# Optimization experiments

Hardware: AMD Instinct MI355X
Metric: run time of the kernel (lower is better)

Reference implementation:

```python
import jax, jax.numpy as jnp
import numpy as np

GAMMA = 0.95        # gamma_lemma: persistence decay per cycle (eq. 12.1)
KAPPA = 0.1         # kappa_interfere: lateral interference strength (eq. 12.3)
T_STEPS = 50        # t_lemma_steps: integration window before selection (eq. 12.2)
FLOOR = 1e-6        # confidence_floor for peak-to-average ratio

B, N_CONCEPTS, N_LEMMAS = 4096, 1024, 512


def setup_inputs() -> dict:
    key = jax.random.key(0)
    k1, k2 = jax.random.split(key, 2)
    # kernel boundary hands in a normalized concept distribution
    c_raw = jax.random.uniform(k1, (B, N_CONCEPTS), dtype=jnp.float32)
    c_lex = c_raw / jnp.sum(c_raw, axis=-1, keepdims=True)
    # TiedSubstrate W_C_to_L: (out_dim=n_lemmas, in_dim=n_concepts)
    W = jax.random.normal(k2, (N_LEMMAS, N_CONCEPTS), dtype=jnp.float32) / np.sqrt(N_CONCEPTS)
    # persistent lemma activation buffer a_lemma, zero at reset
    a0 = jnp.zeros((B, N_LEMMAS), dtype=jnp.float32)
    return {"c_lex": c_lex, "W": W, "a0": a0}


def reference(c_lex, W, a0):
    """Integrate lemma activations for T_STEPS cycles, then select.

    Per cycle (eq. 12.1 + 12.3):
      a <- gamma * a + c_lex @ W^T            # decay + concept->lemma drive
      a <- a - kappa * (sum_j a_j - a)        # lateral interference from other lemmas
      a <- max(a, 0)                          # rectify activations
    Selection (eq. 12.2): argmax over lemmas; confidence = peak / max(mean, floor).
    """
    def step(a, _):
        a = GAMMA * a + jnp.einsum('bc,lc->bl', c_lex, W)   # (B, n_lemmas)
        a = a - KAPPA * (jnp.sum(a, axis=-1, keepdims=True) - a)
        a = jnp.maximum(a, 0.0)
        return a, None

    a, _ = jax.lax.scan(step, a0, None, length=T_STEPS)
    peak = jnp.max(a, axis=-1)
    mean = jnp.mean(a, axis=-1)
    confidence = peak / jnp.maximum(mean, FLOOR)
    selected = jnp.argmax(a, axis=-1)
    return a, selected, confidence
```

## Files before the change

kernel.cpp:

```cpp
#include <hip/hip_runtime.h>
#include <hip/hip_bf16.h>

#define BATCH 4096
#define NC    1024
#define NL    512
#define TSTEPS 50
#define GAMMA_C 0.95f
#define KAPPA_C 0.1f
#define FLOOR_C 1e-6f

typedef __attribute__((ext_vector_type(8))) short short8;
typedef __attribute__((ext_vector_type(4))) float f32x4;

__device__ __forceinline__ void split2_pk(float x0, float x1,
                                          unsigned& hp, unsigned& lp) {
    union { __hip_bfloat162 b; unsigned u; } ch, cl;
    ch.b = __float22bfloat162_rn(make_float2(x0, x1));
    hp = ch.u;
    const float hf0 = __uint_as_float(hp << 16);
    const float hf1 = __uint_as_float(hp & 0xFFFF0000u);
    cl.b = __float22bfloat162_rn(make_float2(x0 - hf0, x1 - hf1));
    lp = cl.u;
}

__device__ __forceinline__ float wave_sum_bcast(float x) {
    float f = x;
    f += __int_as_float(__builtin_amdgcn_update_dpp(
            0, __float_as_int(f), 0x111, 0xf, 0xf, true));
    f += __int_as_float(__builtin_amdgcn_update_dpp(
            0, __float_as_int(f), 0x112, 0xf, 0xf, true));
    f += __int_as_float(__builtin_amdgcn_update_dpp(
            0, __float_as_int(f), 0x114, 0xf, 0xf, true));
    f += __int_as_float(__builtin_amdgcn_update_dpp(
            0, __float_as_int(f), 0x118, 0xf, 0xf, true));
    f += __int_as_float(__builtin_amdgcn_update_dpp(
            0, __float_as_int(f), 0x142, 0xa, 0xf, true));
    f += __int_as_float(__builtin_amdgcn_update_dpp(
            0, __float_as_int(f), 0x143, 0xc, 0xf, true));
    return __int_as_float(__builtin_amdgcn_readlane(__float_as_int(f), 63));
}

__device__ __forceinline__ void glds16f(const float* g, float* l) {
    __builtin_amdgcn_global_load_lds(
        (__attribute__((address_space(1))) void*)(g),
        (__attribute__((address_space(3))) void*)(l), 16, 0, 0);
}

#define TM 128
#define TN 128
#define GK 32
#define SPLITK 4
#define NST (NC / SPLITK / GK)

__global__ __launch_bounds__(256)
void gemm_f32stage(const float* __restrict__ A, const float* __restrict__ W,
                   float* __restrict__ Dp) {
    __shared__ float S[2][2][TM * GK];

    const int tid  = threadIdx.x;
    const int lane = tid & 63;
    const int w    = tid >> 6;

    const int b    = blockIdx.x;
    const int xcd  = b & 7;
    const int slot = b >> 3;
    const int mi_b = xcd * 4 + (slot & 3);
    const int nk   = slot >> 2;
    const int ni_b = nk & 3;
    const int kz   = nk >> 2;

    const int m0 = mi_b * TM;
    const int n0 = ni_b * TN;
    const int kb = kz * (NC / SPLITK);

    const int srow = lane >> 3;
    const int scol = ((lane & 7) * 4) ^ ((srow & 7) << 2);
    const float* gA = A + (size_t)(m0 + w * 32 + srow) * NC + kb + scol;
    const float* gB = W + (size_t)(n0 + w * 32 + srow) * NC + kb + scol;
    const int ldd = (w * 32) * GK;

    const int mw   = (w >> 1) * 64;
    const int nw   = (w & 1) * 64;
    const int sr   = lane & 15;
    const int quad = lane >> 4;
    const int swz = (sr & 7) << 2;
    const int c0  = (quad * 8) ^ swz;
    const int c1  = (quad * 8 + 4) ^ swz;
    const int rAo = (mw + sr) * GK;
    const int rBo = (nw + sr) * GK;

    f32x4 acc[4][4];
    #pragma unroll
    for (int i = 0; i < 4; ++i)
        #pragma unroll
        for (int j = 0; j < 4; ++j)
            acc[i][j] = (f32x4){0.f, 0.f, 0.f, 0.f};

    #define STAGE(buf, kofs)                                               \
        {                                                                  \
            const int ko = (kofs);                                         \
            _Pragma("unroll")                                              \
            for (int c = 0; c < 4; ++c) {                                  \
                glds16f(gA + (size_t)(c * 8) * NC + ko,                    \
                        &S[buf][0][ldd + c * 8 * GK]);                     \
                glds16f(gB + (size_t)(c * 8) * NC + ko,                    \
                        &S[buf][1][ldd + c * 8 * GK]);                     \
            }                                                              \
        }

    #define FRAG(ARR, ROFF, FH, FL)                                        \
        {                                                                  \
            const float4 f0 = *(const float4*)&S[CUR][ARR][(ROFF) + c0];   \
            const float4 f1 = *(const float4*)&S[CUR][ARR][(ROFF) + c1];   \
            uint4 hh, ll;                                                  \
            split2_pk(f0.x, f0.y, hh.x, ll.x);                             \
            split2_pk(f0.z, f0.w, hh.y, ll.y);                             \
            split2_pk(f1.x, f1.y, hh.z, ll.z);                             \
            split2_pk(f1.z, f1.w, hh.w, ll.w);                             \
            FH = *(const short8*)&hh;                                      \
            FL = *(const short8*)&ll;                                      \
        }

    #define KSTEP(CURV, VMSTR, DO_STAGE, NEXTK)                                \
        {                                                                      \
            const int CUR = (CURV);                                            \
            asm volatile("s_waitcnt vmcnt(" VMSTR ")" ::: "memory");           \
            __builtin_amdgcn_sched_barrier(0);                                 \
            __builtin_amdgcn_s_barrier();                                      \
            __builtin_amdgcn_sched_barrier(0);                                 \
            short8 afh[4], afl[4], bfh[4], bfl[4];                             \
            _Pragma("unroll")                                                  \
            for (int mi = 0; mi < 4; ++mi)                                     \
                FRAG(0, rAo + mi * 16 * GK, afh[mi], afl[mi]);                 \
            _Pragma("unroll")                                                  \
            for (int ni = 0; ni < 4; ++ni)                                     \
                FRAG(1, rBo + ni * 16 * GK, bfh[ni], bfl[ni]);                 \
            _Pragma("unroll")                                                  \
            for (int mi = 0; mi < 4; ++mi) {                                   \
                _Pragma("unroll")                                              \
                for (int ni = 0; ni < 4; ++ni) {                               \
                    acc[mi][ni] = __builtin_amdgcn_mfma_f32_16x16x32_bf16(     \
                        afh[mi], bfh[ni], acc[mi][ni], 0, 0, 0);               \
                    acc[mi][ni] = __builtin_amdgcn_mfma_f32_16x16x32_bf16(     \
                        afh[mi], bfl[ni], acc[mi][ni], 0, 0, 0);               \
                    acc[mi][ni] = __builtin_amdgcn_mfma_f32_16x16x32_bf16(     \
                        afl[mi], bfh[ni], acc[mi][ni], 0, 0, 0);               \
                }                                                              \
            }                                                                  \
            __builtin_amdgcn_sched_barrier(0);                                 \
            __builtin_amdgcn_s_barrier();                                      \
            __builtin_amdgcn_sched_barrier(0);                                 \
            if (DO_STAGE) STAGE(CUR, NEXTK);                                   \
        }

    STAGE(0, 0);
    STAGE(1, GK);

    #pragma unroll 2
    for (int s = 0; s < NST - 2; ++s)
        KSTEP((s & 1), "8", true, (s + 2) * GK);
    KSTEP(0, "8", false, 0);
    KSTEP(1, "0", false, 0);

    float* Dz = Dp + (size_t)kz * BATCH * NL;
    #pragma unroll
    for (int mi = 0; mi < 4; ++mi) {
        #pragma unroll
        for (int ni = 0; ni < 4; ++ni) {
            const int col = n0 + nw + ni * 16 + sr;
            #pragma unroll
            for (int r = 0; r < 4; ++r) {
                const int row = m0 + mw + mi * 16 + quad * 4 + r;
                Dz[(size_t)row * NL + col] = acc[mi][ni][r];
            }
        }
    }
}

template<int SK>
__global__ __launch_bounds__(256)
void iterate_select(const float* __restrict__ Dp,
                    float* __restrict__ a_out,
                    float* __restrict__ sel_out, float* __restrict__ conf_out) {
    const int lane = threadIdx.x & 63;
    const int wave = threadIdx.x >> 6;
    const int row  = blockIdx.x * 4 + wave;

    float d[8];
    {
        float4 v[SK][2];
        #pragma unroll
        for (int s = 0; s < SK; ++s) {
            const float4* ps = (const float4*)(Dp + (size_t)s * BATCH * NL
                                               + (size_t)row * NL + lane * 8);
            v[s][0] = ps[0];
            v[s][1] = ps[1];
        }
        d[0] = v[0][0].x; d[1] = v[0][0].y; d[2] = v[0][0].z; d[3] = v[0][0].w;
        d[4] = v[0][1].x; d[5] = v[0][1].y; d[6] = v[0][1].z; d[7] = v[0][1].w;
        #pragma unroll
        for (int s = 1; s < SK; ++s) {
            d[0] += v[s][0].x; d[1] += v[s][0].y; d[2] += v[s][0].z; d[3] += v[s][0].w;
            d[4] += v[s][1].x; d[5] += v[s][1].y; d[6] += v[s][1].z; d[7] += v[s][1].w;
        }
    }

    float a[8];
    #pragma unroll
    for (int j = 0; j < 8; ++j) a[j] = 0.f;

    const float K1 = 1.0f + KAPPA_C;

    for (int t = 0; t < TSTEPS; ++t) {
        #pragma unroll
        for (int j = 0; j < 8; ++j) a[j] = fmaf(GAMMA_C, a[j], d[j]);

        float t4a = a[0] + a[4], t4b = a[1] + a[5], t4c = a[2] + a[6], t4d = a[3] + a[7];
        float t2a = t4a + t4c, t2b = t4b + t4d;
        const float S = wave_sum_bcast(t2a + t2b);

        const float h = -KAPPA_C * S;
        #pragma unroll
        for (int j = 0; j < 8; ++j) {
            const float v = fmaf(K1, a[j], h);
            a[j] = v > 0.f ? v : 0.f;
        }
    }

    float m4a = fmaxf(a[0], a[4]), m4b = fmaxf(a[1], a[5]);
    float m4c = fmaxf(a[2], a[6]), m4d = fmaxf(a[3], a[7]);
    float peak = fmaxf(fmaxf(m4a, m4b), fmaxf(m4c, m4d));
    float s4a = a[0] + a[4], s4b = a[1] + a[5], s4c = a[2] + a[6], s4d = a[3] + a[7];
    float ssum = wave_sum_bcast((s4a + s4b) + (s4c + s4d));

    #pragma unroll
    for (int m = 1; m < 64; m <<= 1)
        peak = fmaxf(peak, __shfl_xor(peak, m, 64));

    const float mean = ssum * (1.0f / (float)NL);
    const float conf = peak / fmaxf(mean, FLOOR_C);

    int idx = 0x7fffffff;
    #pragma unroll
    for (int j = 0; j < 8; ++j)
        if (a[j] == peak) idx = min(idx, lane * 8 + j);
    #pragma unroll
    for (int m = 1; m < 64; m <<= 1)
        idx = min(idx, __shfl_xor(idx, m, 64));

    float4* ar = (float4*)(a_out + (size_t)row * NL + lane * 8);
    float4 o0, o1;
    o0.x = a[0]; o0.y = a[1]; o0.z = a[2]; o0.w = a[3];
    o1.x = a[4]; o1.y = a[5]; o1.z = a[6]; o1.w = a[7];
    ar[0] = o0; ar[1] = o1;

    if (lane == 0) {
        if (sel_out)  sel_out[row]  = (float)idx;
        if (conf_out) conf_out[row] = conf;
    }
}

extern "C" void kernel_launch(void* const* d_in, const int* in_sizes, int n_in,
                              void* d_out, int out_size, void* d_ws, size_t ws_size,
                              hipStream_t stream) {
    const float* c_lex = (const float*)d_in[0];
    const float* W     = (const float*)d_in[1];

    float* D = (float*)d_ws;

    float* a_out = (float*)d_out;
    float* sel   = nullptr;
    float* conf  = nullptr;
    const int base = BATCH * NL;
    if (out_size >= base + 2 * BATCH) {
        sel  = a_out + base;
        conf = a_out + base + BATCH;
    } else if (out_size >= base + BATCH) {
        conf = a_out + base;
    }

    gemm_f32stage<<<dim3(512), 256, 0, stream>>>(c_lex, W, D);

    iterate_select<SPLITK><<<dim3(BATCH / 4), 256, 0, stream>>>(D, a_out, sel, conf);
}
```

Before: 107.9 us.

## Fuse split-K GEMM and iteration into one cooperative kernel with grid sync

Merges the GEMM and the per-row iteration/selection into a single cooperative launch of 512 blocks, separated by a grid-wide sync, so there is one kernel launch instead of two. After the sync each block handles 8 rows, two per wave, instead of the previous 4 rows per block over 1024 blocks. If the cooperative launch fails it falls back to the two-kernel path. The grid sync and the lower row-level parallelism in the second phase (fewer waves in flight for the latency-bound 50-step loop) could offset the saved launch gap.

```diff
diff --git a/kernel.cpp b/kernel.cpp
--- a/kernel.cpp
+++ b/kernel.cpp
@@ -1,5 +1,8 @@
 #include <hip/hip_runtime.h>
 #include <hip/hip_bf16.h>
+#include <hip/hip_cooperative_groups.h>
+
+namespace cg = cooperative_groups;
 
 #define BATCH 4096
 #define NC    1024
@@ -11,6 +14,12 @@
 
 typedef __attribute__((ext_vector_type(8))) short short8;
 typedef __attribute__((ext_vector_type(4))) float f32x4;
+
+#define TM 128
+#define TN 128
+#define GK 32
+#define SPLITK 4
+#define NST (NC / SPLITK / GK)
 
 __device__ __forceinline__ void split2_pk(float x0, float x1,
                                           unsigned& hp, unsigned& lp) {
@@ -46,15 +55,10 @@
         (__attribute__((address_space(3))) void*)(l), 16, 0, 0);
 }
 
-#define TM 128
-#define TN 128
-#define GK 32
-#define SPLITK 4
-#define NST (NC / SPLITK / GK)
-
-__global__ __launch_bounds__(256)
-void gemm_f32stage(const float* __restrict__ A, const float* __restrict__ W,
-                   float* __restrict__ Dp) {
+__device__ __forceinline__ void gemm_phase(const float* __restrict__ A,
+                                           const float* __restrict__ W,
+                                           float* __restrict__ Dp,
+                                           int& mi_b_out, int& slot_out) {
     __shared__ float S[2][2][TM * GK];
 
     const int tid  = threadIdx.x;
@@ -68,6 +72,8 @@
     const int nk   = slot >> 2;
     const int ni_b = nk & 3;
     const int kz   = nk >> 2;
+    mi_b_out = mi_b;
+    slot_out = slot;
 
     const int m0 = mi_b * TM;
     const int n0 = ni_b * TN;
@@ -108,7 +114,7 @@
             }                                                              \
         }
 
-    #define FRAG(ARR, ROFF, FH, FL)                                        \
+    #define FRAG(ARR, ROFF, FH, FL)                                       \
         {                                                                  \
             const float4 f0 = *(const float4*)&S[CUR][ARR][(ROFF) + c0];   \
             const float4 f1 = *(const float4*)&S[CUR][ARR][(ROFF) + c1];   \
@@ -155,12 +161,15 @@
 
     STAGE(0, 0);
     STAGE(1, GK);
-
     #pragma unroll 2
     for (int s = 0; s < NST - 2; ++s)
         KSTEP((s & 1), "8", true, (s + 2) * GK);
     KSTEP(0, "8", false, 0);
     KSTEP(1, "0", false, 0);
+
+    #undef STAGE
+    #undef FRAG
+    #undef KSTEP
 
     float* Dz = Dp + (size_t)kz * BATCH * NL;
     #pragma unroll
@@ -177,7 +186,129 @@
     }
 }
 
-template<int SK>
+template<int NR>
+__device__ __forceinline__ void iterate_rows(const float* __restrict__ Dp,
+                                             const int row0, const int lane,
+                                             float* __restrict__ a_out,
+                                             float* __restrict__ sel_out,
+                                             float* __restrict__ conf_out) {
+    float d[NR][8];
+    #pragma unroll
+    for (int rr = 0; rr < NR; ++rr) {
+        float4 v[SPLITK][2];
+        #pragma unroll
+        for (int s = 0; s < SPLITK; ++s) {
+            const float4* ps = (const float4*)(Dp + (size_t)s * BATCH * NL
+                                               + (size_t)(row0 + rr) * NL + lane * 8);
+            v[s][0] = ps[0];
+            v[s][1] = ps[1];
+        }
+        d[rr][0] = v[0][0].x; d[rr][1] = v[0][0].y; d[rr][2] = v[0][0].z; d[rr][3] = v[0][0].w;
+        d[rr][4] = v[0][1].x; d[rr][5] = v[0][1].y; d[rr][6] = v[0][1].z; d[rr][7] = v[0][1].w;
+        #pragma unroll
+        for (int s = 1; s < SPLITK; ++s) {
+            d[rr][0] += v[s][0].x; d[rr][1] += v[s][0].y; d[rr][2] += v[s][0].z; d[rr][3] += v[s][0].w;
+            d[rr][4] += v[s][1].x; d[rr][5] += v[s][1].y; d[rr][6] += v[s][1].z; d[rr][7] += v[s][1].w;
+        }
+    }
+
+    float a[NR][8];
+    #pragma unroll
+    for (int rr = 0; rr < NR; ++rr)
+        #pragma unroll
+        for (int j = 0; j < 8; ++j) a[rr][j] = 0.f;
+
+    const float K1 = 1.0f + KAPPA_C;
+
+    for (int t = 0; t < TSTEPS; ++t) {
+        #pragma unroll
+        for (int rr = 0; rr < NR; ++rr)
+            #pragma unroll
+            for (int j = 0; j < 8; ++j)
+                a[rr][j] = fmaf(GAMMA_C, a[rr][j], d[rr][j]);
+
+        float S[NR];
+        #pragma unroll
+        for (int rr = 0; rr < NR; ++rr) {
+            float t4a = a[rr][0] + a[rr][4], t4b = a[rr][1] + a[rr][5];
+            float t4c = a[rr][2] + a[rr][6], t4d = a[rr][3] + a[rr][7];
+            float t2a = t4a + t4c, t2b = t4b + t4d;
+            S[rr] = wave_sum_bcast(t2a + t2b);
+        }
+
+        #pragma unroll
+        for (int rr = 0; rr < NR; ++rr) {
+            const float h = -KAPPA_C * S[rr];
+            #pragma unroll
+            for (int j = 0; j < 8; ++j) {
+                const float v = fmaf(K1, a[rr][j], h);
+                a[rr][j] = v > 0.f ? v : 0.f;
+            }
+        }
+    }
+
+    #pragma unroll
+    for (int rr = 0; rr < NR; ++rr) {
+        const int row = row0 + rr;
+        float m4a = fmaxf(a[rr][0], a[rr][4]), m4b = fmaxf(a[rr][1], a[rr][5]);
+        float m4c = fmaxf(a[rr][2], a[rr][6]), m4d = fmaxf(a[rr][3], a[rr][7]);
+        float peak = fmaxf(fmaxf(m4a, m4b), fmaxf(m4c, m4d));
+        float s4a = a[rr][0] + a[rr][4], s4b = a[rr][1] + a[rr][5];
+        float s4c = a[rr][2] + a[rr][6], s4d = a[rr][3] + a[rr][7];
+        float ssum = wave_sum_bcast((s4a + s4b) + (s4c + s4d));
+
+        #pragma unroll
+        for (int m = 1; m < 64; m <<= 1)
+            peak = fmaxf(peak, __shfl_xor(peak, m, 64));
+
+        const float mean = ssum * (1.0f / (float)NL);
+        const float conf = peak / fmaxf(mean, FLOOR_C);
+
+        int idx = 0x7fffffff;
+        #pragma unroll
+        for (int j = 0; j < 8; ++j)
+            if (a[rr][j] == peak) idx = min(idx, lane * 8 + j);
+        #pragma unroll
+        for (int m = 1; m < 64; m <<= 1)
+            idx = min(idx, __shfl_xor(idx, m, 64));
+
+        float4 o0, o1;
+        o0.x = a[rr][0]; o0.y = a[rr][1]; o0.z = a[rr][2]; o0.w = a[rr][3];
+        o1.x = a[rr][4]; o1.y = a[rr][5]; o1.z = a[rr][6]; o1.w = a[rr][7];
+        float4* arp = (float4*)(a_out + (size_t)row * NL + lane * 8);
+        arp[0] = o0; arp[1] = o1;
+
+        if (lane == 0) {
+            if (sel_out)  sel_out[row]  = (float)idx;
+            if (conf_out) conf_out[row] = conf;
+        }
+    }
+}
+
+__global__ __launch_bounds__(256)
+void fused_gi(const float* __restrict__ A, const float* __restrict__ W,
+              float* __restrict__ D, float* __restrict__ a_out,
+              float* __restrict__ sel_out, float* __restrict__ conf_out) {
+    int mi_b, slot;
+    gemm_phase(A, W, D, mi_b, slot);
+
+    __threadfence();
+    cg::this_grid().sync();
+
+    const int lane = threadIdx.x & 63;
+    const int w    = threadIdx.x >> 6;
+    const int nk2  = slot >> 2;
+    const int row0 = mi_b * 128 + nk2 * 8 + w * 2;
+    iterate_rows<2>(D, row0, lane, a_out, sel_out, conf_out);
+}
+
+__global__ __launch_bounds__(256)
+void gemm_f32stage(const float* __restrict__ A, const float* __restrict__ W,
+                   float* __restrict__ Dp) {
+    int mi_b, slot;
+    gemm_phase(A, W, Dp, mi_b, slot);
+}
+
 __global__ __launch_bounds__(256)
 void iterate_select(const float* __restrict__ Dp,
                     float* __restrict__ a_out,
@@ -185,79 +316,7 @@
     const int lane = threadIdx.x & 63;
     const int wave = threadIdx.x >> 6;
     const int row  = blockIdx.x * 4 + wave;
-
-    float d[8];
-    {
-        float4 v[SK][2];
-        #pragma unroll
-        for (int s = 0; s < SK; ++s) {
-            const float4* ps = (const float4*)(Dp + (size_t)s * BATCH * NL
-                                               + (size_t)row * NL + lane * 8);
-            v[s][0] = ps[0];
-            v[s][1] = ps[1];
-        }
-        d[0] = v[0][0].x; d[1] = v[0][0].y; d[2] = v[0][0].z; d[3] = v[0][0].w;
-        d[4] = v[0][1].x; d[5] = v[0][1].y; d[6] = v[0][1].z; d[7] = v[0][1].w;
-        #pragma unroll
-        for (int s = 1; s < SK; ++s) {
-            d[0] += v[s][0].x; d[1] += v[s][0].y; d[2] += v[s][0].z; d[3] += v[s][0].w;
-            d[4] += v[s][1].x; d[5] += v[s][1].y; d[6] += v[s][1].z; d[7] += v[s][1].w;
-        }
-    }
-
-    float a[8];
-    #pragma unroll
-    for (int j = 0; j < 8; ++j) a[j] = 0.f;
-
-    const float K1 = 1.0f + KAPPA_C;
-
-    for (int t = 0; t < TSTEPS; ++t) {
-        #pragma unroll
-        for (int j = 0; j < 8; ++j) a[j] = fmaf(GAMMA_C, a[j], d[j]);
-
-        float t4a = a[0] + a[4], t4b = a[1] + a[5], t4c = a[2] + a[6], t4d = a[3] + a[7];
-        float t2a = t4a + t4c, t2b = t4b + t4d;
-        const float S = wave_sum_bcast(t2a + t2b);
-
-        const float h = -KAPPA_C * S;
-        #pragma unroll
-        for (int j = 0; j < 8; ++j) {
-            const float v = fmaf(K1, a[j], h);
-            a[j] = v > 0.f ? v : 0.f;
-        }
-    }
-
-    float m4a = fmaxf(a[0], a[4]), m4b = fmaxf(a[1], a[5]);
-    float m4c = fmaxf(a[2], a[6]), m4d = fmaxf(a[3], a[7]);
-    float peak = fmaxf(fmaxf(m4a, m4b), fmaxf(m4c, m4d));
-    float s4a = a[0] + a[4], s4b = a[1] + a[5], s4c = a[2] + a[6], s4d = a[3] + a[7];
-    float ssum = wave_sum_bcast((s4a + s4b) + (s4c + s4d));
-
-    #pragma unroll
-    for (int m = 1; m < 64; m <<= 1)
-        peak = fmaxf(peak, __shfl_xor(peak, m, 64));
-
-    const float mean = ssum * (1.0f / (float)NL);
-    const float conf = peak / fmaxf(mean, FLOOR_C);
-
-    int idx = 0x7fffffff;
-    #pragma unroll
-    for (int j = 0; j < 8; ++j)
-        if (a[j] == peak) idx = min(idx, lane * 8 + j);
-    #pragma unroll
-    for (int m = 1; m < 64; m <<= 1)
-        idx = min(idx, __shfl_xor(idx, m, 64));
-
-    float4* ar = (float4*)(a_out + (size_t)row * NL + lane * 8);
-    float4 o0, o1;
-    o0.x = a[0]; o0.y = a[1]; o0.z = a[2]; o0.w = a[3];
-    o1.x = a[4]; o1.y = a[5]; o1.z = a[6]; o1.w = a[7];
-    ar[0] = o0; ar[1] = o1;
-
-    if (lane == 0) {
-        if (sel_out)  sel_out[row]  = (float)idx;
-        if (conf_out) conf_out[row] = conf;
-    }
+    iterate_rows<1>(Dp, row, lane, a_out, sel_out, conf_out);
 }
 
 extern "C" void kernel_launch(void* const* d_in, const int* in_sizes, int n_in,
@@ -279,7 +338,13 @@
         conf = a_out + base;
     }
 
-    gemm_f32stage<<<dim3(512), 256, 0, stream>>>(c_lex, W, D);
-
-    iterate_select<SPLITK><<<dim3(BATCH / 4), 256, 0, stream>>>(D, a_out, sel, conf);
-}
+    void* args[] = {(void*)&c_lex, (void*)&W, (void*)&D,
+                    (void*)&a_out, (void*)&sel, (void*)&conf};
+    hipError_t e = hipLaunchCooperativeKernel((const void*)fused_gi,
+                                              dim3(512), dim3(256),
+                                              args, 0, stream);
+    if (e != hipSuccess) {
+        gemm_f32stage<<<dim3(512), 256, 0, stream>>>(c_lex, W, D);
+        iterate_select<<<dim3(BATCH / 4), 256, 0, stream>>>(D, a_out, sel, conf);
+    }
+}
```

New measurement: 248.3 us. 2.3x slower.
